# Performance work log

Measured on AMD Instinct MI355X. Metric: run time of the kernel, lower is better.

The kernel has to match this reference:

```python
import jax, jax.numpy as jnp
import numpy as np

FEAT = 512      # feat_dim
HID = 256       # feat_dim // 2
K = 4           # DSL knn k
NCLS = 2
BUF = 8192      # rehearsal buffer size
B_BAGS = 8
N_INST = 16384


def _lin_init(k, i, o):
    return jax.random.normal(k, (i, o), jnp.float32) / np.sqrt(i)


def setup_inputs() -> dict:
    key = jax.random.key(0)
    ks = jax.random.split(key, 16)
    p = {}
    p['x'] = jax.random.normal(ks[0], (B_BAGS, N_INST, FEAT), jnp.float32)
    p['rehearsal'] = jax.random.uniform(ks[1], (BUF, FEAT), jnp.float32)
    # attention MIL pooling MLP
    p['aW1'] = _lin_init(ks[2], FEAT, FEAT); p['ab1'] = jnp.zeros((FEAT,), jnp.float32)
    p['aW2'] = _lin_init(ks[3], FEAT, 1);    p['ab2'] = jnp.zeros((1,), jnp.float32)
    # bag classifier
    p['cW'] = _lin_init(ks[4], FEAT, NCLS);  p['cb'] = jnp.zeros((NCLS,), jnp.float32)
    # DSL fc
    p['dW1'] = _lin_init(ks[5], FEAT, HID);  p['db1'] = jnp.zeros((HID,), jnp.float32)
    p['dW2'] = _lin_init(ks[6], HID, FEAT);  p['db2'] = jnp.zeros((FEAT,), jnp.float32)
    # GCN: hgc1 / hgc2 (HypergraphConv, heads=1, use_attention)
    p['g1W'] = _lin_init(ks[7], FEAT, FEAT)
    p['g1att'] = jax.random.normal(ks[8], (2 * FEAT,), jnp.float32) * 0.05
    p['g1b'] = jnp.zeros((FEAT,), jnp.float32)
    p['n1w'] = jnp.ones((FEAT,), jnp.float32); p['n1b'] = jnp.zeros((FEAT,), jnp.float32); p['n1s'] = jnp.ones((FEAT,), jnp.float32)
    p['f1W'] = _lin_init(ks[9], FEAT, HID);  p['f1b'] = jnp.zeros((HID,), jnp.float32)
    p['g2W'] = _lin_init(ks[10], FEAT, FEAT)
    p['g2att'] = jax.random.normal(ks[11], (2 * FEAT,), jnp.float32) * 0.05
    p['g2b'] = jnp.zeros((FEAT,), jnp.float32)
    p['n2w'] = jnp.ones((FEAT,), jnp.float32); p['n2b'] = jnp.zeros((FEAT,), jnp.float32); p['n2s'] = jnp.ones((FEAT,), jnp.float32)
    p['f2W'] = _lin_init(ks[12], FEAT, HID); p['f2b'] = jnp.zeros((HID,), jnp.float32)
    p['clW'] = _lin_init(ks[13], HID, NCLS); p['clb'] = jnp.zeros((NCLS,), jnp.float32)
    return p


def _hconv(x, eattr, src, edst, W, att, bias, n):
    """PyG HypergraphConv, heads=1, use_attention=True, concat, dropout=0.
    src = hyperedge_index[0] (node ids), edst = hyperedge_index[1] (hyperedge ids)."""
    xs = x @ W            # [n, F] node features after lin
    ea = eattr @ W        # [n, F] hyperedge attrs after lin
    F = xs.shape[1]
    alpha = xs[src] @ att[:F] + ea[edst] @ att[F:]        # [E]
    alpha = jax.nn.leaky_relu(alpha, 0.2)
    # softmax grouped by node index (hyperedge_index[0])
    m = jax.ops.segment_max(alpha, src, num_segments=n)
    e = jnp.exp(alpha - m[src])
    s = jax.ops.segment_sum(e, src, num_segments=n)
    alpha = e / s[src]
    ones = jnp.ones_like(alpha)
    deg = jax.ops.segment_sum(ones, src, num_segments=n)   # node degree D
    Dinv = jnp.where(deg > 0, 1.0 / deg, 0.0)
    esz = jax.ops.segment_sum(ones, edst, num_segments=n)  # hyperedge size B
    Binv = jnp.where(esz > 0, 1.0 / esz, 0.0)
    # node -> hyperedge, then hyperedge -> node
    out_e = jax.ops.segment_sum((Binv[edst] * alpha)[:, None] * xs[src], edst, num_segments=n)
    out_n = jax.ops.segment_sum((Dinv[src] * alpha)[:, None] * out_e[edst], src, num_segments=n)
    return out_n + bias


def _gnorm(x, w, b, s, eps=1e-5):
    # PyG GraphNorm, single graph
    mu = jnp.mean(x, axis=0)
    o = x - mu * s
    var = jnp.mean(o * o, axis=0)
    return w * o / jnp.sqrt(var + eps) + b


def reference(x, rehearsal, aW1, ab1, aW2, ab2, cW, cb, dW1, db1, dW2, db2,
              g1W, g1att, g1b, n1w, n1b, n1s, f1W, f1b,
              g2W, g2att, g2b, n2w, n2b, n2s, f2W, f2b, clW, clb):
    B = x.shape[0]
    # attention MIL pooling
    h = jax.nn.relu(x @ aW1 + ab1)                 # [B, N, F]
    scores = (h @ aW2 + ab2)[..., 0]               # [B, N]
    A = jax.nn.softmax(scores, axis=-1)
    M = jnp.einsum('bn,bnd->bd', A, x)             # [B, F]
    logits_mlp = M @ cW + cb
    # concat with rehearsal buffer -> graph nodes
    xc = jnp.concatenate([M, rehearsal], axis=0)   # [B+BUF, F]
    # DSL fc
    xg = jax.nn.leaky_relu(xc @ dW1 + db1, 0.01)
    xg = jax.nn.leaky_relu(xg @ dW2 + db2, 0.01)
    n = xg.shape[0]
    # cosine KNN (includes self, as torch_cluster.knn(x, x))
    xn = xg / (jnp.linalg.norm(xg, axis=1, keepdims=True) + 1e-12)
    sim = xn @ xn.T                                 # [n, n]
    _, nbr = jax.lax.top_k(sim, K)                  # [n, K]
    src = nbr.reshape(-1)                           # neighbor node ids
    edst = jnp.repeat(jnp.arange(n), K)             # hyperedge ids (query nodes)
    # scatter_mean of neighbor features per hyperedge (each has exactly K members)
    eattr = jnp.mean(xg[nbr], axis=1)               # [n, F]
    # GCN with hypergraph convs
    x1 = _hconv(xg, eattr, src, edst, g1W, g1att, g1b, n)
    x1 = jax.nn.leaky_relu(_gnorm(x1, n1w, n1b, n1s), 0.01)
    out = jax.nn.leaky_relu(x1 @ f1W + f1b, 0.01)
    x2 = _hconv(x1, eattr, src, edst, g2W, g2att, g2b, n)
    x2 = jax.nn.leaky_relu(_gnorm(x2, n2w, n2b, n2s), 0.01)
    out = out + jax.nn.leaky_relu(x2 @ f2W + f2b, 0.01)
    logits = out @ clW + clb
    logits_graph = logits[:B]
    return logits_mlp, logits_graph
```

## Files before the change

kernel.cpp:

```cpp
#include <hip/hip_runtime.h>
#include <math.h>
#include <limits.h>

#define FDIM 512
#define HIDN 256
#define NBAGS 8
#define NINST 16384
#define NNODE 8200
#define NEDGE 32800
#define BFSPLIT 16
#define SPLITW 513
#define MCHUNK 128

typedef __attribute__((ext_vector_type(8))) short short8v;
typedef __attribute__((ext_vector_type(4))) float f32x4v;

__device__ __forceinline__ float lrelu(float v, float s){ return v >= 0.f ? v : v*s; }

__device__ __forceinline__ void ins4(float v, int id, float* tv, int* ti){
    if ((v > tv[3]) || (v == tv[3] && id < ti[3])){
        tv[3]=v; ti[3]=id;
#pragma unroll
        for (int q=3;q>0;--q){
            bool sw = (tv[q] > tv[q-1]) || (tv[q]==tv[q-1] && ti[q]<ti[q-1]);
            if (sw){ float f=tv[q]; tv[q]=tv[q-1]; tv[q-1]=f; int d=ti[q]; ti[q]=ti[q-1]; ti[q-1]=d; }
        }
    }
}

__device__ __forceinline__ void ins8(float v, int id, float* tv, int* ti){
    if ((v > tv[7]) || (v == tv[7] && id < ti[7])){
        tv[7]=v; ti[7]=id;
#pragma unroll
        for (int q=7;q>0;--q){
            bool sw = (tv[q] > tv[q-1]) || (tv[q]==tv[q-1] && ti[q]<ti[q-1]);
            if (sw){ float f=tv[q]; tv[q]=tv[q-1]; tv[q-1]=f; int d=ti[q]; ti[q]=ti[q-1]; ti[q-1]=d; }
        }
    }
}

__device__ __forceinline__ unsigned short f2bf(float f){
    unsigned u = __float_as_uint(f);
    unsigned r = u + 0x7FFFu + ((u >> 16) & 1u);
    return (unsigned short)(r >> 16);
}
__device__ __forceinline__ float bf2f(unsigned short h){
    return __uint_as_float((unsigned)h << 16);
}

__global__ void k_wsplit(const float* __restrict__ W,
        unsigned short* __restrict__ WThi, unsigned short* __restrict__ WTlo){
    int i = blockIdx.x*256 + threadIdx.x;
    int k = i >> 9, n = i & 511;
    float w = W[i];
    unsigned short hi = f2bf(w);
    unsigned short lo = f2bf(w - bf2f(hi));
    WThi[(size_t)n*512 + k] = hi;
    WTlo[(size_t)n*512 + k] = lo;
}

__global__ __launch_bounds__(256) void k_scores(const float* __restrict__ X,
        const unsigned short* __restrict__ WThi, const unsigned short* __restrict__ WTlo,
        const float* __restrict__ b1, const float* __restrict__ v2,
        float* __restrict__ scoresP)
{
    __shared__ unsigned short Ahi[128][40];
    __shared__ unsigned short Alo[128][40];
    __shared__ unsigned short Bhi[128][40];
    __shared__ unsigned short Blo[128][40];
    int t = threadIdx.x;
    int wv = t >> 6, lane = t & 63;
    int lcol = lane & 15, lk = lane >> 4;
    size_t mb = (size_t)blockIdx.y * 128;
    int nb = blockIdx.x * 128;

    f32x4v acc[2][8];
#pragma unroll
    for (int rf=0;rf<2;rf++)
#pragma unroll
        for (int cf=0;cf<8;cf++) acc[rf][cf] = (f32x4v){0.f,0.f,0.f,0.f};

    for (int kc = 0; kc < 512; kc += 32){
        __syncthreads();
#pragma unroll
        for (int q=0;q<4;q++){
            int idx = q*256 + t;
            int seg = idx & 7, row = idx >> 3;
            float4 v = *(const float4*)(X + (mb+row)*512 + kc + seg*4);
            ushort4 h, l;
            h.x=f2bf(v.x); h.y=f2bf(v.y); h.z=f2bf(v.z); h.w=f2bf(v.w);
            l.x=f2bf(v.x-bf2f(h.x)); l.y=f2bf(v.y-bf2f(h.y));
            l.z=f2bf(v.z-bf2f(h.z)); l.w=f2bf(v.w-bf2f(h.w));
            *(ushort4*)&Ahi[row][seg*4] = h;
            *(ushort4*)&Alo[row][seg*4] = l;
        }
#pragma unroll
        for (int q=0;q<2;q++){
            int idx = q*256 + t;
            int col = idx >> 2, part = idx & 3;
            *(short8v*)&Bhi[col][part*8] =
                *(const short8v*)(WThi + (size_t)(nb+col)*512 + kc + part*8);
            *(short8v*)&Blo[col][part*8] =
                *(const short8v*)(WTlo + (size_t)(nb+col)*512 + kc + part*8);
        }
        __syncthreads();
        int r0 = wv*32;
        short8v ah0 = *(const short8v*)&Ahi[r0      + lcol][lk*8];
        short8v al0 = *(const short8v*)&Alo[r0      + lcol][lk*8];
        short8v ah1 = *(const short8v*)&Ahi[r0 + 16 + lcol][lk*8];
        short8v al1 = *(const short8v*)&Alo[r0 + 16 + lcol][lk*8];
#pragma unroll
        for (int cf=0; cf<8; cf++){
            short8v bh = *(const short8v*)&Bhi[cf*16 + lcol][lk*8];
            short8v bl = *(const short8v*)&Blo[cf*16 + lcol][lk*8];
            acc[0][cf] = __builtin_amdgcn_mfma_f32_16x16x32_bf16(ah0, bh, acc[0][cf], 0,0,0);
            acc[0][cf] = __builtin_amdgcn_mfma_f32_16x16x32_bf16(ah0, bl, acc[0][cf], 0,0,0);
            acc[0][cf] = __builtin_amdgcn_mfma_f32_16x16x32_bf16(al0, bh, acc[0][cf], 0,0,0);
            acc[1][cf] = __builtin_amdgcn_mfma_f32_16x16x32_bf16(ah1, bh, acc[1][cf], 0,0,0);
            acc[1][cf] = __builtin_amdgcn_mfma_f32_16x16x32_bf16(ah1, bl, acc[1][cf], 0,0,0);
            acc[1][cf] = __builtin_amdgcn_mfma_f32_16x16x32_bf16(al1, bh, acc[1][cf], 0,0,0);
        }
    }
    float rowsum[2][4];
#pragma unroll
    for (int rf=0;rf<2;rf++)
#pragma unroll
        for (int r=0;r<4;r++) rowsum[rf][r]=0.f;
#pragma unroll
    for (int rf=0; rf<2; rf++)
#pragma unroll
        for (int cf=0; cf<8; cf++){
            int gc = nb + cf*16 + lcol;
            float bb = b1[gc], vv = v2[gc];
#pragma unroll
            for (int r=0;r<4;r++){
                float h = acc[rf][cf][r] + bb;
                h = h > 0.f ? h : 0.f;
                rowsum[rf][r] = fmaf(h, vv, rowsum[rf][r]);
            }
        }
#pragma unroll
    for (int mask=1; mask<16; mask<<=1)
#pragma unroll
        for (int rf=0;rf<2;rf++)
#pragma unroll
            for (int r=0;r<4;r++)
                rowsum[rf][r] += __shfl_xor(rowsum[rf][r], mask);
    if (lcol == 0){
#pragma unroll
        for (int rf=0;rf<2;rf++)
#pragma unroll
            for (int r=0;r<4;r++){
                size_t grow = mb + wv*32 + rf*16 + lk*4 + r;
                scoresP[(size_t)blockIdx.x*(NBAGS*NINST) + grow] = rowsum[rf][r];
            }
    }
}

__global__ __launch_bounds__(256) void k_gemm3(const float* __restrict__ X,
        const unsigned short* __restrict__ WThi, const unsigned short* __restrict__ WTlo,
        const float* __restrict__ bias, float* __restrict__ C,
        int M, int N, int K, float slope)
{
    __shared__ unsigned short Ahi[128][40];
    __shared__ unsigned short Alo[128][40];
    __shared__ unsigned short Bhi[128][40];
    __shared__ unsigned short Blo[128][40];
    int t = threadIdx.x;
    int wv = t >> 6, lane = t & 63;
    int lcol = lane & 15, lk = lane >> 4;
    int mb = blockIdx.y * 128;
    int nb = blockIdx.x * 128;

    f32x4v acc[2][8];
#pragma unroll
    for (int rf=0;rf<2;rf++)
#pragma unroll
        for (int cf=0;cf<8;cf++) acc[rf][cf] = (f32x4v){0.f,0.f,0.f,0.f};

    for (int kc = 0; kc < K; kc += 32){
        __syncthreads();
#pragma unroll
        for (int q=0;q<4;q++){
            int idx = q*256 + t;
            int seg = idx & 7, row = idx >> 3;
            int gr = mb + row; if (gr >= M) gr = M-1;
            float4 v = *(const float4*)(X + (size_t)gr*K + kc + seg*4);
            ushort4 h, l;
            h.x=f2bf(v.x); h.y=f2bf(v.y); h.z=f2bf(v.z); h.w=f2bf(v.w);
            l.x=f2bf(v.x-bf2f(h.x)); l.y=f2bf(v.y-bf2f(h.y));
            l.z=f2bf(v.z-bf2f(h.z)); l.w=f2bf(v.w-bf2f(h.w));
            *(ushort4*)&Ahi[row][seg*4] = h;
            *(ushort4*)&Alo[row][seg*4] = l;
        }
#pragma unroll
        for (int q=0;q<2;q++){
            int idx = q*256 + t;
            int col = idx >> 2, part = idx & 3;
            *(short8v*)&Bhi[col][part*8] =
                *(const short8v*)(WThi + (size_t)(nb+col)*K + kc + part*8);
            *(short8v*)&Blo[col][part*8] =
                *(const short8v*)(WTlo + (size_t)(nb+col)*K + kc + part*8);
        }
        __syncthreads();
        int r0 = wv*32;
        short8v ah0 = *(const short8v*)&Ahi[r0      + lcol][lk*8];
        short8v al0 = *(const short8v*)&Alo[r0      + lcol][lk*8];
        short8v ah1 = *(const short8v*)&Ahi[r0 + 16 + lcol][lk*8];
        short8v al1 = *(const short8v*)&Alo[r0 + 16 + lcol][lk*8];
#pragma unroll
        for (int cf=0; cf<8; cf++){
            short8v bh = *(const short8v*)&Bhi[cf*16 + lcol][lk*8];
            short8v bl = *(const short8v*)&Blo[cf*16 + lcol][lk*8];
            acc[0][cf] = __builtin_amdgcn_mfma_f32_16x16x32_bf16(ah0, bh, acc[0][cf], 0,0,0);
            acc[0][cf] = __builtin_amdgcn_mfma_f32_16x16x32_bf16(ah0, bl, acc[0][cf], 0,0,0);
            acc[0][cf] = __builtin_amdgcn_mfma_f32_16x16x32_bf16(al0, bh, acc[0][cf], 0,0,0);
            acc[1][cf] = __builtin_amdgcn_mfma_f32_16x16x32_bf16(ah1, bh, acc[1][cf], 0,0,0);
            acc[1][cf] = __builtin_amdgcn_mfma_f32_16x16x32_bf16(ah1, bl, acc[1][cf], 0,0,0);
            acc[1][cf] = __builtin_amdgcn_mfma_f32_16x16x32_bf16(al1, bh, acc[1][cf], 0,0,0);
        }
    }
#pragma unroll
    for (int rf=0; rf<2; rf++)
#pragma unroll
        for (int cf=0; cf<8; cf++){
            int gc = nb + cf*16 + lcol;
            float bb = bias ? bias[gc] : 0.f;
#pragma unroll
            for (int r=0;r<4;r++){
                int grow = mb + wv*32 + rf*16 + lk*4 + r;
                if (grow < M){
                    float v = acc[rf][cf][r] + bb;
                    C[(size_t)grow*N + gc] = lrelu(v, slope);
                }
            }
        }
}

__global__ void k_scred(const float* __restrict__ sp, float* __restrict__ s){
    int r = blockIdx.x*256+threadIdx.x;
    if (r < NBAGS*NINST)
        s[r] = sp[r] + sp[NBAGS*NINST + r] + sp[2*NBAGS*NINST + r] + sp[3*NBAGS*NINST + r];
}

__global__ __launch_bounds__(256) void k_softmax(float* __restrict__ s0){
    int b = blockIdx.x; float* s = s0 + (size_t)b*NINST;
    __shared__ float red[256];
    int t = threadIdx.x;
    float m = -INFINITY;
    for (int i=t;i<NINST;i+=256) m = fmaxf(m, s[i]);
    red[t]=m; __syncthreads();
    for (int st=128; st>0; st>>=1){ if(t<st) red[t]=fmaxf(red[t],red[t+st]); __syncthreads(); }
    m = red[0]; __syncthreads();
    float sum=0.f;
    for (int i=t;i<NINST;i+=256) sum += __expf(s[i]-m);
    red[t]=sum; __syncthreads();
    for (int st=128; st>0; st>>=1){ if(t<st) red[t]+=red[t+st]; __syncthreads(); }
    float inv = 1.f/red[0];
    for (int i=t;i<NINST;i+=256) s[i] = __expf(s[i]-m)*inv;
}

__global__ __launch_bounds__(256) void k_M(const float* __restrict__ x,
        const float* __restrict__ A, float* __restrict__ MP){
    int b = blockIdx.y; int chunk = blockIdx.x;
    int n0 = chunk*(NINST/MCHUNK);
    __shared__ float As[NINST/MCHUNK];
    int t=threadIdx.x;
    if (t < NINST/MCHUNK) As[t] = A[(size_t)b*NINST+n0+t];
    __syncthreads();
    float a0=0.f, a1=0.f;
    const float* xb = x + ((size_t)b*NINST + n0)*FDIM;
    for (int n=0;n<NINST/MCHUNK;n++){
        float w = As[n];
        a0 = fmaf(w, xb[(size_t)n*FDIM + t],       a0);
        a1 = fmaf(w, xb[(size_t)n*FDIM + t + 256], a1);
    }
    MP[((size_t)chunk*NBAGS + b)*FDIM + t]       = a0;
    MP[((size_t)chunk*NBAGS + b)*FDIM + t + 256] = a1;
}

__global__ void k_Mred(const float* __restrict__ mp, float* __restrict__ M_){
    int b = blockIdx.x; int d = threadIdx.x;
    float s=0.f;
    for (int c=0;c<MCHUNK;c++) s += mp[((size_t)c*NBAGS+b)*FDIM + d];
    M_[b*FDIM+d]=s;
}

__global__ void k_logits_mlp(const float* __restrict__ M_, const float* __restrict__ cW,
        const float* __restrict__ cb, float* __restrict__ outp){
    int t = threadIdx.x;
    if (t < 16){
        int r=t>>1, c=t&1;
        float s=cb[c];
        for (int k=0;k<FDIM;k++) s = fmaf(M_[r*FDIM+k], cW[k*2+c], s);
        outp[r*2+c] = s;
    }
}

__global__ void k_xc(const float* __restrict__ M_, const float* __restrict__ reh, float* __restrict__ xc){
    size_t i = (size_t)blockIdx.x*256 + threadIdx.x;
    if (i >= (size_t)NNODE*FDIM) return;
    xc[i] = (i < (size_t)NBAGS*FDIM) ? M_[i] : reh[i - (size_t)NBAGS*FDIM];
}

__global__ __launch_bounds__(256) void k_gemm(const float* __restrict__ X,
        const float* __restrict__ W, const float* __restrict__ bias,
        float* __restrict__ C, unsigned short* __restrict__ Cbf,
        int M, int N, int K, float slope)
{
    __shared__ float As[32][68];
    __shared__ float Ws[32][128];
    int t = threadIdx.x; int tx = t & 15, ty = t >> 4;
    int mb = blockIdx.y * 64, nb = blockIdx.x * 128;
    float acc[4][8];
#pragma unroll
    for (int i=0;i<4;i++)
#pragma unroll
        for (int j=0;j<8;j++) acc[i][j]=0.f;

    int kq=(t&7)*4, m0=t>>3;
    int n4=(t&31)*4, k0=t>>5;
    for (int kc=0;kc<K;kc+=32){
#pragma unroll
        for (int mm=0;mm<2;mm++){
            int m = m0 + mm*32;
            int gr = mb + m; if (gr >= M) gr = M-1;
            float4 v = *(const float4*)(X + (size_t)gr*K + kc + kq);
            As[kq+0][m]=v.x; As[kq+1][m]=v.y; As[kq+2][m]=v.z; As[kq+3][m]=v.w;
        }
#pragma unroll
        for (int kk=0;kk<4;kk++){
            float4 v = *(const float4*)(W + (size_t)(kc+k0+kk*8)*N + nb + n4);
            *(float4*)&Ws[k0+kk*8][n4] = v;
        }
        __syncthreads();
#pragma unroll 4
        for (int k=0;k<32;k++){
            float4 a = *(const float4*)&As[k][ty*4];
            float4 b0 = *(const float4*)&Ws[k][tx*4];
            float4 b1 = *(const float4*)&Ws[k][64+tx*4];
            float av[4]={a.x,a.y,a.z,a.w};
            float bv[8]={b0.x,b0.y,b0.z,b0.w,b1.x,b1.y,b1.z,b1.w};
#pragma unroll
            for (int i=0;i<4;i++)
#pragma unroll
                for (int j=0;j<8;j++)
                    acc[i][j] = fmaf(av[i], bv[j], acc[i][j]);
        }
        __syncthreads();
    }
#pragma unroll
    for (int i=0;i<4;i++){
        int gr = mb + ty*4 + i;
        if (gr >= M) continue;
        float o[8];
#pragma unroll
        for (int j=0;j<8;j++){
            int gc = (j<4) ? (nb + tx*4 + j) : (nb + 64 + tx*4 + (j-4));
            float v = acc[i][j] + (bias ? bias[gc] : 0.f);
            o[j] = lrelu(v, slope);
        }
        float4 o0 = make_float4(o[0],o[1],o[2],o[3]);
        float4 o1 = make_float4(o[4],o[5],o[6],o[7]);
        *(float4*)(C + (size_t)gr*N + nb + tx*4)      = o0;
        *(float4*)(C + (size_t)gr*N + nb + 64 + tx*4) = o1;
        if (Cbf){
            ushort4 h0, h1;
            h0.x=f2bf(o[0]); h0.y=f2bf(o[1]); h0.z=f2bf(o[2]); h0.w=f2bf(o[3]);
            h1.x=f2bf(o[4]); h1.y=f2bf(o[5]); h1.z=f2bf(o[6]); h1.w=f2bf(o[7]);
            *(ushort4*)(Cbf + (size_t)gr*N + nb + tx*4)      = h0;
            *(ushort4*)(Cbf + (size_t)gr*N + nb + 64 + tx*4) = h1;
        }
    }
}

__global__ void k_rowdot(const float* __restrict__ X, const float* __restrict__ v,
        float* __restrict__ out, int K, int mode){
    int r = blockIdx.x; int t = threadIdx.x;
    const float* xr = X + (size_t)r*K;
    float s = 0.f;
    if (mode==1){ for (int k=t;k<K;k+=64){ float x_=xr[k]; s=fmaf(x_,x_,s);} }
    else        { for (int k=t;k<K;k+=64) s=fmaf(xr[k],v[k],s); }
    for (int off=32;off;off>>=1) s += __shfl_down(s, off);
    if (t==0) out[r] = (mode==1)? 1.f/(sqrtf(s)+1e-12f) : s;
}

__global__ void k_watt(const float* __restrict__ W, const float* __restrict__ att2, float* __restrict__ w2){
    int k = blockIdx.x; int t=threadIdx.x;
    float s=0.f;
    for (int j=t;j<FDIM;j+=64) s=fmaf(W[(size_t)k*FDIM+j], att2[j], s);
    for (int off=32;off;off>>=1) s += __shfl_down(s, off);
    if (t==0) w2[k]=s;
}

__global__ __launch_bounds__(256) void k_simbf(const unsigned short* __restrict__ xgh,
        const float* __restrict__ rn, float* __restrict__ candV, int* __restrict__ candI)
{
    __shared__ unsigned short Bs[16][520];
    int t = threadIdx.x;
    int wv = t >> 6, lane = t & 63;
    int lcol = lane & 15, lk = lane >> 4;
    int split = blockIdx.x;
    int r0 = blockIdx.y * 64 + wv * 16;

    short8v aF[16];
    {
        int arow = r0 + lcol; if (arow >= NNODE) arow = NNODE - 1;
        const unsigned short* ap = xgh + (size_t)arow * FDIM + lk * 8;
#pragma unroll
        for (int s = 0; s < 16; s++)
            aF[s] = *(const short8v*)(ap + s * 32);
    }

    int c0 = split * SPLITW;
    int cend = c0 + SPLITW; if (cend > NNODE) cend = NNODE;

    float tv[4][4]; int ti[4][4];
#pragma unroll
    for (int i=0;i<4;i++)
#pragma unroll
        for (int q=0;q<4;q++){ tv[i][q]=-INFINITY; ti[i][q]=INT_MAX; }

    int rho = t >> 4, seg = t & 15;

    for (int cc = c0; cc < cend; cc += 16){
        __syncthreads();
        {
            int gc = cc + rho; if (gc >= cend) gc = cend - 1;
            const unsigned short* bp = xgh + (size_t)gc * FDIM;
#pragma unroll
            for (int p = 0; p < 4; p++)
                *(short8v*)&Bs[rho][seg*8 + p*128] = *(const short8v*)(bp + seg*8 + p*128);
        }
        __syncthreads();

        f32x4v acc0 = {0.f,0.f,0.f,0.f};
        f32x4v acc1 = {0.f,0.f,0.f,0.f};
#pragma unroll
        for (int s = 0; s < 8; s++){
            short8v b0 = *(const short8v*)&Bs[lcol][lk*8 + s*32];
            short8v b1 = *(const short8v*)&Bs[lcol][lk*8 + (s+8)*32];
            acc0 = __builtin_amdgcn_mfma_f32_16x16x32_bf16(aF[s],   b0, acc0, 0, 0, 0);
            acc1 = __builtin_amdgcn_mfma_f32_16x16x32_bf16(aF[s+8], b1, acc1, 0, 0, 0);
        }
        int gcol = cc + lcol;
        bool valid = gcol < cend;
        float rnc = valid ? rn[gcol] : 0.f;
#pragma unroll
        for (int i = 0; i < 4; i++){
            float v = valid ? (acc0[i] + acc1[i]) * rnc : -INFINITY;
            ins4(v, gcol, tv[i], ti[i]);
        }
    }

    float mv[4][8]; int mi[4][8];
#pragma unroll
    for (int i=0;i<4;i++){
#pragma unroll
        for (int q=0;q<4;q++){ mv[i][q]=tv[i][q]; mi[i][q]=ti[i][q]; }
#pragma unroll
        for (int q=4;q<8;q++){ mv[i][q]=-INFINITY; mi[i][q]=INT_MAX; }
    }
#pragma unroll
    for (int mask=1; mask<16; mask<<=1){
        float ov[4][8]; int oi[4][8];
#pragma unroll
        for (int i=0;i<4;i++)
#pragma unroll
            for (int q=0;q<8;q++){
                ov[i][q] = __shfl_xor(mv[i][q], mask);
                oi[i][q] = __shfl_xor(mi[i][q], mask);
            }
#pragma unroll
        for (int i=0;i<4;i++)
#pragma unroll
            for (int q=0;q<8;q++)
                ins8(ov[i][q], oi[i][q], mv[i], mi[i]);
    }
    if (lcol == 0){
#pragma unroll
        for (int i=0;i<4;i++){
            int grow = r0 + lk*4 + i;
            if (grow < NNODE){
#pragma unroll
                for (int q=0;q<8;q++){
                    candV[((size_t)grow*BFSPLIT + split)*8 + q] = mv[i][q];
                    candI[((size_t)grow*BFSPLIT + split)*8 + q] = mi[i][q];
                }
            }
        }
    }
}

__global__ __launch_bounds__(256) void k_rescore(const float* __restrict__ xg,
        const float* __restrict__ rn, const float* __restrict__ candV,
        const int* __restrict__ candI, int half,
        float* __restrict__ htV, int* __restrict__ htI)
{
    __shared__ float Xr[4][512];
    __shared__ float Cs[256][17];
    __shared__ int   CrowS[256];
    int t = threadIdx.x;
    int wv = t >> 6, lane = t & 63;
    int r0 = blockIdx.x * 4;
    int r  = r0 + wv;
    int cid = candI[(size_t)r*128 + half*64 + lane];
    float pv = candV[(size_t)r*128 + half*64 + lane];
    bool ok = (pv != -INFINITY) && (cid >= 0) && (cid < NNODE);
    int crow = ok ? cid : 0;
    CrowS[t] = crow;
    {
        int rr = t >> 6; int c = t & 63;
        const float* xp = xg + (size_t)(r0+rr)*FDIM;
        *(float4*)&Xr[rr][c*4]       = *(const float4*)(xp + c*4);
        *(float4*)&Xr[rr][256 + c*4] = *(const float4*)(xp + 256 + c*4);
    }
    float dot = 0.f;
    for (int kc = 0; kc < 512; kc += 16){
        __syncthreads();
#pragma unroll
        for (int p = 0; p < 4; p++){
            int slot = p*64 + (t >> 2);
            int f = t & 3;
            float4 v = *(const float4*)(xg + (size_t)CrowS[slot]*FDIM + kc + f*4);
            float* dst = &Cs[slot][f*4];
            dst[0]=v.x; dst[1]=v.y; dst[2]=v.z; dst[3]=v.w;
        }
        __syncthreads();
#pragma unroll
        for (int k2 = 0; k2 < 16; k2++)
            dot = fmaf(Xr[wv][kc + k2], Cs[t][k2], dot);
    }
    float v = ok ? (dot * rn[r]) * rn[crow] : -INFINITY;
    int id = ok ? cid : INT_MAX;
    float tvv[4]={-INFINITY,-INFINITY,-INFINITY,-INFINITY};
    int tii[4]={INT_MAX,INT_MAX,INT_MAX,INT_MAX};
    ins4(v, id, tvv, tii);
#pragma unroll
    for (int mask=1; mask<64; mask<<=1){
        float ov[4]; int oi[4];
#pragma unroll
        for (int s=0;s<4;s++){ ov[s]=__shfl_xor(tvv[s],mask); oi[s]=__shfl_xor(tii[s],mask); }
#pragma unroll
        for (int s=0;s<4;s++) ins4(ov[s], oi[s], tvv, tii);
    }
    if (lane == 0){
#pragma unroll
        for (int s=0;s<4;s++){ htV[r*8 + half*4 + s] = tvv[s]; htI[r*8 + half*4 + s] = tii[s]; }
    }
}

__global__ void k_hmerge(const float* __restrict__ htV, const int* __restrict__ htI,
        int* __restrict__ nbr){
    int r = blockIdx.x*256+threadIdx.x; if (r>=NNODE) return;
    float tv[4]={-INFINITY,-INFINITY,-INFINITY,-INFINITY};
    int ti[4]={INT_MAX,INT_MAX,INT_MAX,INT_MAX};
#pragma unroll
    for (int q=0;q<8;q++) ins4(htV[r*8+q], htI[r*8+q], tv, ti);
#pragma unroll
    for (int s=0;s<4;s++) nbr[r*4+s] = ti[s];
}

__global__ void k_eattr(const float* __restrict__ xg, const int* __restrict__ nbr, float* __restrict__ ea){
    int j = blockIdx.x; int t = threadIdx.x;
    int n0=nbr[j*4], n1=nbr[j*4+1], n2=nbr[j*4+2], n3=nbr[j*4+3];
    for (int d=t; d<FDIM; d+=256){
        float s = xg[(size_t)n0*FDIM+d]+xg[(size_t)n1*FDIM+d]+xg[(size_t)n2*FDIM+d]+xg[(size_t)n3*FDIM+d];
        ea[(size_t)j*FDIM+d] = 0.25f*s;
    }
}

__global__ void k_count(const int* __restrict__ nbr, int* __restrict__ counts){
    int e = blockIdx.x*256+threadIdx.x; if(e<NEDGE) atomicAdd(&counts[nbr[e]],1);
}

__global__ void k_scan(const int* __restrict__ counts, int* __restrict__ csrOff){
    __shared__ int part[257];
    int t=threadIdx.x;
    int start = t*33; int s=0;
    for (int i=0;i<33;i++){ int idx=start+i; if(idx<NNODE) s += counts[idx]; }
    part[t+1]=s; if(t==0) part[0]=0;
    __syncthreads();
    if (t==0){ for (int i=1;i<=256;i++) part[i]+=part[i-1]; }
    __syncthreads();
    int run = part[t];
    for (int i=0;i<33;i++){ int idx=start+i; if(idx<NNODE){ csrOff[idx]=run; run+=counts[idx]; } }
    if (t==255) csrOff[NNODE]=run;
}

__global__ void k_fill(const int* __restrict__ nbr, const int* __restrict__ csrOff,
        int* __restrict__ fillPos, int* __restrict__ csrE){
    int e = blockIdx.x*256+threadIdx.x; if(e>=NEDGE) return;
    int i = nbr[e];
    int p = atomicAdd(&fillPos[i],1);
    csrE[csrOff[i]+p] = e;
}

__global__ void k_alpha(const int* __restrict__ nbr, const float* __restrict__ ps,
        const float* __restrict__ pe, float* __restrict__ alphan){
    int e = blockIdx.x*256+threadIdx.x; if(e>=NEDGE) return;
    float a = ps[nbr[e]] + pe[e>>2];
    alphan[e] = a>=0.f? a : 0.2f*a;
}

__global__ void k_esm(const int* __restrict__ csrOff, const int* __restrict__ csrE,
        float* __restrict__ alphan){
    int i = blockIdx.x*256+threadIdx.x; if(i>=NNODE) return;
    int s0=csrOff[i], s1=csrOff[i+1];
    if (s1==s0) return;
    float m=-INFINITY;
    for (int s=s0;s<s1;s++) m = fmaxf(m, alphan[csrE[s]]);
    float Z=0.f;
    for (int s=s0;s<s1;s++) Z += __expf(alphan[csrE[s]]-m);
    float inv = 1.f/Z;
    for (int s=s0;s<s1;s++){ int e=csrE[s]; alphan[e] = __expf(alphan[e]-m)*inv; }
}

__global__ void k_oute(const float* __restrict__ xs, const float* __restrict__ alphan,
        const int* __restrict__ nbr, float* __restrict__ out_e){
    int j = blockIdx.x; int t=threadIdx.x;
    __shared__ float a[4]; __shared__ int sidx[4];
    if (t<4){ a[t]=alphan[j*4+t]; sidx[t]=nbr[j*4+t]; }
    __syncthreads();
    for (int d=t; d<FDIM; d+=256){
        float v = a[0]*xs[(size_t)sidx[0]*FDIM+d] + a[1]*xs[(size_t)sidx[1]*FDIM+d]
                + a[2]*xs[(size_t)sidx[2]*FDIM+d] + a[3]*xs[(size_t)sidx[3]*FDIM+d];
        out_e[(size_t)j*FDIM+d] = 0.25f*v;
    }
}

__global__ void k_outn(const float* __restrict__ out_e, const float* __restrict__ alphan,
        const int* __restrict__ csrOff, const int* __restrict__ csrE,
        const float* __restrict__ bias, float* __restrict__ out_n){
    int i = blockIdx.x; int t=threadIdx.x;
    int s0=csrOff[i], s1=csrOff[i+1];
    float Dinv = (s1>s0)? 1.f/(float)(s1-s0) : 0.f;
    for (int d=t; d<FDIM; d+=256){
        float accv=0.f;
        for (int s=s0;s<s1;s++){
            int e=csrE[s];
            accv = fmaf(alphan[e], out_e[(size_t)(e>>2)*FDIM+d], accv);
        }
        out_n[(size_t)i*FDIM+d] = bias[d] + Dinv*accv;
    }
}

__global__ void k_colstat1(const float* __restrict__ Xn, float* __restrict__ p1, float* __restrict__ p2){
    int b = blockIdx.x; int t=threadIdx.x;
    float s0=0,q0=0,s1=0,q1=0;
    for (int r=b; r<NNODE; r+=64){
        float v0 = Xn[(size_t)r*FDIM + t];
        float v1 = Xn[(size_t)r*FDIM + t + 256];
        s0+=v0; q0=fmaf(v0,v0,q0); s1+=v1; q1=fmaf(v1,v1,q1);
    }
    p1[b*FDIM+t]=s0; p1[b*FDIM+t+256]=s1;
    p2[b*FDIM+t]=q0; p2[b*FDIM+t+256]=q1;
}

__global__ void k_colstat2(const float* __restrict__ p1, const float* __restrict__ p2,
        const float* __restrict__ w, const float* __restrict__ sc,
        float* __restrict__ mu, float* __restrict__ g){
    int d = threadIdx.x + blockIdx.x*256; if(d>=FDIM) return;
    float s=0,q=0;
    for (int bb=0;bb<64;bb++){ s+=p1[bb*FDIM+d]; q+=p2[bb*FDIM+d]; }
    float m = s/(float)NNODE;
    float ms = m*sc[d];
    float var = q/(float)NNODE - 2.f*ms*m + ms*ms;
    mu[d]=m;
    g[d] = w[d]*rsqrtf(var+1e-5f);
}

__global__ void k_gnapply(const float* __restrict__ Xin, const float* __restrict__ mu,
        const float* __restrict__ g, const float* __restrict__ sc,
        const float* __restrict__ bb, float* __restrict__ Xout){
    size_t i = (size_t)blockIdx.x*256+threadIdx.x;
    if (i >= (size_t)NNODE*FDIM) return;
    int d = (int)(i & 511);
    float o = Xin[i] - mu[d]*sc[d];
    Xout[i] = lrelu(g[d]*o + bb[d], 0.01f);
}

__global__ void k_final(const float* __restrict__ x1, const float* __restrict__ x2,
        const float* __restrict__ f1W, const float* __restrict__ f1b,
        const float* __restrict__ f2W, const float* __restrict__ f2b,
        const float* __restrict__ clW, const float* __restrict__ clb,
        float* __restrict__ outp){
    int r = blockIdx.x;
    int h = threadIdx.x;
    __shared__ float o8[HIDN];
    float s1=f1b[h], s2=f2b[h];
    for (int k=0;k<FDIM;k++){
        s1 = fmaf(x1[(size_t)r*FDIM+k], f1W[(size_t)k*HIDN+h], s1);
        s2 = fmaf(x2[(size_t)r*FDIM+k], f2W[(size_t)k*HIDN+h], s2);
    }
    o8[h] = lrelu(s1,0.01f)+lrelu(s2,0.01f);
    __syncthreads();
    if (h < 2){
        float s = clb[h];
        for (int k=0;k<HIDN;k++) s = fmaf(o8[k], clW[k*2+h], s);
        outp[16 + r*2 + h] = s;
    }
}

extern "C" void kernel_launch(void* const* d_in, const int* in_sizes, int n_in,
                              void* d_out, int out_size, void* d_ws, size_t ws_size,
                              hipStream_t stream) {
    (void)in_sizes; (void)n_in; (void)out_size; (void)ws_size;
    const float* x    = (const float*)d_in[0];
    const float* reh  = (const float*)d_in[1];
    const float* aW1  = (const float*)d_in[2];
    const float* ab1  = (const float*)d_in[3];
    const float* aW2  = (const float*)d_in[4];
    const float* cW   = (const float*)d_in[6];
    const float* cb   = (const float*)d_in[7];
    const float* dW1  = (const float*)d_in[8];
    const float* db1  = (const float*)d_in[9];
    const float* dW2  = (const float*)d_in[10];
    const float* db2  = (const float*)d_in[11];
    const float* g1W  = (const float*)d_in[12];
    const float* g1att= (const float*)d_in[13];
    const float* g1b  = (const float*)d_in[14];
    const float* n1w  = (const float*)d_in[15];
    const float* n1b  = (const float*)d_in[16];
    const float* n1s  = (const float*)d_in[17];
    const float* f1W  = (const float*)d_in[18];
    const float* f1b  = (const float*)d_in[19];
    const float* g2W  = (const float*)d_in[20];
    const float* g2att= (const float*)d_in[21];
    const float* g2b  = (const float*)d_in[22];
    const float* n2w  = (const float*)d_in[23];
    const float* n2b  = (const float*)d_in[24];
    const float* n2s  = (const float*)d_in[25];
    const float* f2W  = (const float*)d_in[26];
    const float* f2b  = (const float*)d_in[27];
    const float* clW  = (const float*)d_in[28];
    const float* clb  = (const float*)d_in[29];
    float* out = (float*)d_out;
    char* ws = (char*)d_ws;

    float* scores = (float*)(ws + 0);
    float* Mbuf   = (float*)(ws + 524288);
    float* xc     = (float*)(ws + 540672);
    float* xg1    = (float*)(ws + 17334272);
    float* xg     = (float*)(ws + 25731072);
    float* rn     = (float*)(ws + 42524672);
    int*   nbrp   = (int*)  (ws + 44656896);
    float* eattr  = (float*)(ws + 44788224);
    int*   counts = (int*)  (ws + 61581824);
    int*   csrOff = (int*)  (ws + 61614848);
    int*   fillPos= (int*)  (ws + 61647872);
    int*   csrE   = (int*)  (ws + 61680896);
    float* w2     = (float*)(ws + 61812096);
    float* ps     = (float*)(ws + 61814144);
    float* pe     = (float*)(ws + 61847040);
    float* alphan = (float*)(ws + 61880064);
    float* out_e  = (float*)(ws + 62011264);
    float* out_n  = (float*)(ws + 78804864);
    float* part1  = (float*)(ws + 95598464);
    float* part2  = (float*)(ws + 95729536);
    float* mu     = (float*)(ws + 95860608);
    float* gsc    = (float*)(ws + 95862656);
    float* x1buf  = (float*)(ws + 95864704);
    float* scoresP= (float*)(ws + 112658304);
    float* xs     = xc;
    float* x2buf  = xg;
    float* MP     = scoresP;
    unsigned short* gW1hi = (unsigned short*)scoresP;
    unsigned short* gW1lo = (unsigned short*)((char*)scoresP + 524288);
    unsigned short* gW2hi = (unsigned short*)((char*)scoresP + 1048576);
    unsigned short* gW2lo = (unsigned short*)((char*)scoresP + 1572864);
    unsigned short* WThi = (unsigned short*)eattr;
    unsigned short* WTlo = (unsigned short*)((char*)eattr + 524288);
    unsigned short* xgh = (unsigned short*)out_e;
    int*   candI = (int*)((char*)out_e + 8396800);
    int*   htI   = (int*)((char*)out_e + 12595200);
    float* candV = out_n;
    float* htV   = (float*)((char*)out_n + 4198400);

    hipMemsetAsync(counts, 0, NNODE*sizeof(int), stream);
    hipMemsetAsync(fillPos, 0, NNODE*sizeof(int), stream);

    k_wsplit<<<1024,256,0,stream>>>(aW1, WThi, WTlo);
    k_scores<<<dim3(4,1024),256,0,stream>>>(x, WThi, WTlo, ab1, aW2, scoresP);
    k_scred<<<512,256,0,stream>>>(scoresP, scores);
    k_softmax<<<NBAGS,256,0,stream>>>(scores);
    k_M<<<dim3(MCHUNK,NBAGS),256,0,stream>>>(x, scores, MP);
    k_Mred<<<NBAGS,512,0,stream>>>(MP, Mbuf);
    k_logits_mlp<<<1,64,0,stream>>>(Mbuf, cW, cb, out);

    k_wsplit<<<1024,256,0,stream>>>(g1W, gW1hi, gW1lo);
    k_wsplit<<<1024,256,0,stream>>>(g2W, gW2hi, gW2lo);

    k_xc<<<(NNODE*FDIM+255)/256,256,0,stream>>>(Mbuf, reh, xc);
    k_gemm<<<dim3(2,(NNODE+63)/64),256,0,stream>>>(xc, dW1, db1, xg1, nullptr, NNODE, HIDN, FDIM, 0.01f);
    k_gemm<<<dim3(4,(NNODE+63)/64),256,0,stream>>>(xg1, dW2, db2, xg, xgh, NNODE, FDIM, HIDN, 0.01f);

    k_rowdot<<<NNODE,64,0,stream>>>(xg, nullptr, rn, FDIM, 1);
    k_simbf<<<dim3(BFSPLIT,(NNODE+63)/64),256,0,stream>>>(xgh, rn, candV, candI);
    k_rescore<<<NNODE/4,256,0,stream>>>(xg, rn, candV, candI, 0, htV, htI);
    k_rescore<<<NNODE/4,256,0,stream>>>(xg, rn, candV, candI, 1, htV, htI);
    k_hmerge<<<(NNODE+255)/256,256,0,stream>>>(htV, htI, nbrp);
    k_eattr<<<NNODE,256,0,stream>>>(xg, nbrp, eattr);
    k_count<<<(NEDGE+255)/256,256,0,stream>>>(nbrp, counts);
    k_scan<<<1,256,0,stream>>>(counts, csrOff);
    k_fill<<<(NEDGE+255)/256,256,0,stream>>>(nbrp, csrOff, fillPos, csrE);

    for (int layer=0; layer<2; ++layer){
        const float* Xin  = layer==0 ? xg   : x1buf;
        const float* W    = layer==0 ? g1W  : g2W;
        const unsigned short* Whi = layer==0 ? gW1hi : gW2hi;
        const unsigned short* Wlo = layer==0 ? gW1lo : gW2lo;
        const float* att  = layer==0 ? g1att: g2att;
        const float* gb   = layer==0 ? g1b  : g2b;
        const float* nw   = layer==0 ? n1w  : n2w;
        const float* nb_  = layer==0 ? n1b  : n2b;
        const float* ns   = layer==0 ? n1s  : n2s;
        float* Xout       = layer==0 ? x1buf: x2buf;

        k_gemm3<<<dim3(4,(NNODE+127)/128),256,0,stream>>>(Xin, Whi, Wlo, nullptr, xs, NNODE, FDIM, FDIM, 1.0f);
        k_watt<<<FDIM,64,0,stream>>>(W, att+FDIM, w2);
        k_rowdot<<<NNODE,64,0,stream>>>(xs, att, ps, FDIM, 0);
        k_rowdot<<<NNODE,64,0,stream>>>(eattr, w2, pe, FDIM, 0);
        k_alpha<<<(NEDGE+255)/256,256,0,stream>>>(nbrp, ps, pe, alphan);
        k_esm<<<(NNODE+255)/256,256,0,stream>>>(csrOff, csrE, alphan);
        k_oute<<<NNODE,256,0,stream>>>(xs, alphan, nbrp, out_e);
        k_outn<<<NNODE,256,0,stream>>>(out_e, alphan, csrOff, csrE, gb, out_n);
        k_colstat1<<<64,256,0,stream>>>(out_n, part1, part2);
        k_colstat2<<<2,256,0,stream>>>(part1, part2, nw, ns, mu, gsc);
        k_gnapply<<<(NNODE*FDIM+255)/256,256,0,stream>>>(out_n, mu, gsc, ns, nb_, Xout);
    }

    k_final<<<NBAGS,HIDN,0,stream>>>(x1buf, x2buf, f1W, f1b, f2W, f2b, clW, clb, out);
}
```

Before: 1.654 ms.

## Load MFMA operands directly from global memory, dropping LDS staging in scores and sim kernels

In k_scores and k_simbf, the shared-memory tiles and their __syncthreads barriers are removed. Each wave now loads its A and B MFMA fragments straight from global memory (through cache) into registers. In k_scores the hi/lo bf16 split of X is done per lane in registers. This cuts barrier and LDS traffic, but B tiles are now fetched redundantly by all four waves, and A is split redundantly across the column blocks. It relies on L1/L2 hits, and the global loads are uncoalesced strided 16-byte accesses.

```diff
diff --git a/kernel.cpp b/kernel.cpp
--- a/kernel.cpp
+++ b/kernel.cpp
@@ -48,6 +48,16 @@
     return __uint_as_float((unsigned)h << 16);
 }
 
+__device__ __forceinline__ void split8(float4 a, float4 b, short8v& h8, short8v& l8){
+    float v[8] = {a.x,a.y,a.z,a.w,b.x,b.y,b.z,b.w};
+#pragma unroll
+    for (int j=0;j<8;j++){
+        unsigned short hi = f2bf(v[j]);
+        h8[j] = (short)hi;
+        l8[j] = (short)f2bf(v[j] - bf2f(hi));
+    }
+}
+
 __global__ void k_wsplit(const float* __restrict__ W,
         unsigned short* __restrict__ WThi, unsigned short* __restrict__ WTlo){
     int i = blockIdx.x*256 + threadIdx.x;
@@ -64,10 +74,6 @@
         const float* __restrict__ b1, const float* __restrict__ v2,
         float* __restrict__ scoresP)
 {
-    __shared__ unsigned short Ahi[128][40];
-    __shared__ unsigned short Alo[128][40];
-    __shared__ unsigned short Bhi[128][40];
-    __shared__ unsigned short Blo[128][40];
     int t = threadIdx.x;
     int wv = t >> 6, lane = t & 63;
     int lcol = lane & 15, lk = lane >> 4;
@@ -80,39 +86,22 @@
 #pragma unroll
         for (int cf=0;cf<8;cf++) acc[rf][cf] = (f32x4v){0.f,0.f,0.f,0.f};
 
+    const float* pA0 = X + (mb + wv*32 + lcol)*512 + lk*8;
+    const float* pA1 = pA0 + 16*512;
+
     for (int kc = 0; kc < 512; kc += 32){
-        __syncthreads();
-#pragma unroll
-        for (int q=0;q<4;q++){
-            int idx = q*256 + t;
-            int seg = idx & 7, row = idx >> 3;
-            float4 v = *(const float4*)(X + (mb+row)*512 + kc + seg*4);
-            ushort4 h, l;
-            h.x=f2bf(v.x); h.y=f2bf(v.y); h.z=f2bf(v.z); h.w=f2bf(v.w);
-            l.x=f2bf(v.x-bf2f(h.x)); l.y=f2bf(v.y-bf2f(h.y));
-            l.z=f2bf(v.z-bf2f(h.z)); l.w=f2bf(v.w-bf2f(h.w));
-            *(ushort4*)&Ahi[row][seg*4] = h;
-            *(ushort4*)&Alo[row][seg*4] = l;
-        }
-#pragma unroll
-        for (int q=0;q<2;q++){
-            int idx = q*256 + t;
-            int col = idx >> 2, part = idx & 3;
-            *(short8v*)&Bhi[col][part*8] =
-                *(const short8v*)(WThi + (size_t)(nb+col)*512 + kc + part*8);
-            *(short8v*)&Blo[col][part*8] =
-                *(const short8v*)(WTlo + (size_t)(nb+col)*512 + kc + part*8);
-        }
-        __syncthreads();
-        int r0 = wv*32;
-        short8v ah0 = *(const short8v*)&Ahi[r0      + lcol][lk*8];
-        short8v al0 = *(const short8v*)&Alo[r0      + lcol][lk*8];
-        short8v ah1 = *(const short8v*)&Ahi[r0 + 16 + lcol][lk*8];
-        short8v al1 = *(const short8v*)&Alo[r0 + 16 + lcol][lk*8];
+        float4 a0a = *(const float4*)(pA0 + kc);
+        float4 a0b = *(const float4*)(pA0 + kc + 4);
+        float4 a1a = *(const float4*)(pA1 + kc);
+        float4 a1b = *(const float4*)(pA1 + kc + 4);
+        short8v ah0, al0, ah1, al1;
+        split8(a0a, a0b, ah0, al0);
+        split8(a1a, a1b, ah1, al1);
 #pragma unroll
         for (int cf=0; cf<8; cf++){
-            short8v bh = *(const short8v*)&Bhi[cf*16 + lcol][lk*8];
-            short8v bl = *(const short8v*)&Blo[cf*16 + lcol][lk*8];
+            size_t coff = (size_t)(nb + cf*16 + lcol)*512 + kc + lk*8;
+            short8v bh = *(const short8v*)(WThi + coff);
+            short8v bl = *(const short8v*)(WTlo + coff);
             acc[0][cf] = __builtin_amdgcn_mfma_f32_16x16x32_bf16(ah0, bh, acc[0][cf], 0,0,0);
             acc[0][cf] = __builtin_amdgcn_mfma_f32_16x16x32_bf16(ah0, bl, acc[0][cf], 0,0,0);
             acc[0][cf] = __builtin_amdgcn_mfma_f32_16x16x32_bf16(al0, bh, acc[0][cf], 0,0,0);
@@ -396,7 +385,6 @@
 __global__ __launch_bounds__(256) void k_simbf(const unsigned short* __restrict__ xgh,
         const float* __restrict__ rn, float* __restrict__ candV, int* __restrict__ candI)
 {
-    __shared__ unsigned short Bs[16][520];
     int t = threadIdx.x;
     int wv = t >> 6, lane = t & 63;
     int lcol = lane & 15, lk = lane >> 4;
@@ -421,25 +409,16 @@
 #pragma unroll
         for (int q=0;q<4;q++){ tv[i][q]=-INFINITY; ti[i][q]=INT_MAX; }
 
-    int rho = t >> 4, seg = t & 15;
-
     for (int cc = c0; cc < cend; cc += 16){
-        __syncthreads();
-        {
-            int gc = cc + rho; if (gc >= cend) gc = cend - 1;
-            const unsigned short* bp = xgh + (size_t)gc * FDIM;
-#pragma unroll
-            for (int p = 0; p < 4; p++)
-                *(short8v*)&Bs[rho][seg*8 + p*128] = *(const short8v*)(bp + seg*8 + p*128);
-        }
-        __syncthreads();
+        int gc = cc + lcol; if (gc >= cend) gc = cend - 1;
+        const unsigned short* bp = xgh + (size_t)gc * FDIM + lk * 8;
 
         f32x4v acc0 = {0.f,0.f,0.f,0.f};
         f32x4v acc1 = {0.f,0.f,0.f,0.f};
 #pragma unroll
         for (int s = 0; s < 8; s++){
-            short8v b0 = *(const short8v*)&Bs[lcol][lk*8 + s*32];
-            short8v b1 = *(const short8v*)&Bs[lcol][lk*8 + (s+8)*32];
+            short8v b0 = *(const short8v*)(bp + s*32);
+            short8v b1 = *(const short8v*)(bp + (s+8)*32);
             acc0 = __builtin_amdgcn_mfma_f32_16x16x32_bf16(aF[s],   b0, acc0, 0, 0, 0);
             acc1 = __builtin_amdgcn_mfma_f32_16x16x32_bf16(aF[s+8], b1, acc1, 0, 0, 0);
         }
```

New measurement: 2.292 ms. 38.5% more time.
